# Kernel tuning notes

Hardware: AMD Instinct MI355X
Metric: run time of the kernel (lower is better)

## Reference

```python
import jax, jax.numpy as jnp
import numpy as np

B, S, DK = 32, 2048, 64

def setup_inputs() -> dict:
    key = jax.random.key(0)
    kq, kk, kv = jax.random.split(key, 3)
    Q = jax.random.normal(kq, (B, S, DK), dtype=jnp.float32)
    K = jax.random.normal(kk, (B, S, DK), dtype=jnp.float32)
    V = jax.random.normal(kv, (B, S, DK), dtype=jnp.float32)
    return {"Q": Q, "K": K, "V": V}

def reference(Q, K, V):
    # attn_scores = Q K^T / sqrt(d_k); full [B,S,S] probs materialized (naive, non-flash)
    d_k = Q.shape[-1]
    scores = jnp.einsum('bqd,bkd->bqk', Q, K) / jnp.sqrt(jnp.asarray(d_k, Q.dtype))
    probs = jax.nn.softmax(scores, axis=-1)
    return jnp.einsum('bqk,bkd->bqd', probs, V)
```

## Files before the change

kernel.cpp:

```cpp
#include <hip/hip_runtime.h>
#include <hip/hip_bf16.h>

#define BATCH 32
#define SEQ   2048
#define DKK   64

constexpr int QT  = 128;
constexpr int KT  = 64;
constexpr int NIT = SEQ / KT;
constexpr int LST = 66;

typedef __attribute__((ext_vector_type(8)))  short bf16x8;
typedef __attribute__((ext_vector_type(16))) float f32x16;
typedef __attribute__((ext_vector_type(2)))  unsigned uint2v;

__device__ __forceinline__ unsigned cvt2(float a, float b) {
    union { __hip_bfloat162 h; unsigned u; } c;
    c.h = __float22bfloat162_rn(make_float2(a, b));
    return c.u;
}

__device__ __forceinline__ float fast_exp2(float x) {
#if __has_builtin(__builtin_amdgcn_exp2f)
    return __builtin_amdgcn_exp2f(x);
#else
    return exp2f(x);
#endif
}

__global__ __launch_bounds__(256, 2) void attn_fwd(
        const float* __restrict__ Q, const float* __restrict__ K,
        const float* __restrict__ V, float* __restrict__ O) {
    __shared__ short Kb[2][KT][LST];
    __shared__ short Vt[2][DKK][LST];

    const int tid  = threadIdx.x;
    const int w    = tid >> 6;
    const int lane = tid & 63;
    const int hi   = lane >> 5;
    const int l31  = lane & 31;

    const int lin  = (int)blockIdx.x + ((int)blockIdx.y << 4);
    const int work = ((lin & 7) << 6) | (lin >> 3);
    const int b    = work >> 4;
    const int q0   = (work & 15) * QT + w * 32;

    const float qscale = 0.125f * 1.44269504088896340736f;
    bf16x8 qfrag[4];
    #pragma unroll
    for (int c = 0; c < 4; ++c) {
        const float* qp = Q + ((size_t)b * SEQ + q0 + l31) * DKK + 16*c + 8*hi;
        float4 a  = *(const float4*)qp;
        float4 a2 = *(const float4*)(qp + 4);
        union { bf16x8 v; unsigned u[4]; } f;
        f.u[0] = cvt2(a.x*qscale,  a.y*qscale);
        f.u[1] = cvt2(a.z*qscale,  a.w*qscale);
        f.u[2] = cvt2(a2.x*qscale, a2.y*qscale);
        f.u[3] = cvt2(a2.z*qscale, a2.w*qscale);
        qfrag[c] = f.v;
    }

    f32x16 o0 = {}, o1 = {};
    float ls0 = 0.f, ls1 = 0.f, ls2 = 0.f, ls3 = 0.f;

    const float* Kbase = K + (size_t)b * SEQ * DKK;
    const float* Vbase = V + (size_t)b * SEQ * DKK;

    const int krow0 = tid >> 4;
    const int kcol  = (tid & 15) << 2;
    const int vd    = tid & 63;
    const int vg    = (tid >> 6) << 4;

    float4 kp[4];
    float  vp[16];
    auto load_regs = [&](int t) {
        const float* Kg = Kbase + (size_t)(t * KT) * DKK;
        #pragma unroll
        for (int i = 0; i < 4; ++i)
            kp[i] = *(const float4*)(Kg + (size_t)(krow0 + 16*i) * DKK + kcol);
        const float* Vg = Vbase + (size_t)(t * KT + vg) * DKK + vd;
        #pragma unroll
        for (int i = 0; i < 16; ++i) vp[i] = Vg[(size_t)i * DKK];
    };
    auto write_lds = [&](int buf) {
        #pragma unroll
        for (int i = 0; i < 4; ++i) {
            int2 kk;
            kk.x = (int)cvt2(kp[i].x, kp[i].y);
            kk.y = (int)cvt2(kp[i].z, kp[i].w);
            *(int2*)&Kb[buf][krow0 + 16*i][kcol] = kk;
        }
        union { bf16x8 v; unsigned u[4]; } t0, t1;
        t0.u[0] = cvt2(vp[0],  vp[1]);  t0.u[1] = cvt2(vp[2],  vp[3]);
        t0.u[2] = cvt2(vp[4],  vp[5]);  t0.u[3] = cvt2(vp[6],  vp[7]);
        t1.u[0] = cvt2(vp[8],  vp[9]);  t1.u[1] = cvt2(vp[10], vp[11]);
        t1.u[2] = cvt2(vp[12], vp[13]); t1.u[3] = cvt2(vp[14], vp[15]);
        *(bf16x8*)&Vt[buf][vd][vg]     = t0.v;
        *(bf16x8*)&Vt[buf][vd][vg + 8] = t1.v;
    };

    load_regs(0);
    write_lds(0);
    load_regs(1);
    __syncthreads();

    for (int it = 0; it < NIT; ++it) {
        const int cur = it & 1;

        #pragma unroll
        for (int kt2 = 0; kt2 < 2; ++kt2) {
            f32x16 acc = {};
            __builtin_amdgcn_s_setprio(1);
            #pragma unroll
            for (int c = 0; c < 4; ++c) {
                bf16x8 kf = *(const bf16x8*)&Kb[cur][32*kt2 + l31][16*c + 8*hi];
                acc = __builtin_amdgcn_mfma_f32_32x32x16_bf16(kf, qfrag[c], acc, 0, 0, 0);
            }
            __builtin_amdgcn_s_setprio(0);

            float p[16];
            #pragma unroll
            for (int r = 0; r < 16; r += 4) {
                p[r]   = fast_exp2(acc[r]);   ls0 += p[r];
                p[r+1] = fast_exp2(acc[r+1]); ls1 += p[r+1];
                p[r+2] = fast_exp2(acc[r+2]); ls2 += p[r+2];
                p[r+3] = fast_exp2(acc[r+3]); ls3 += p[r+3];
            }

            unsigned pw0 = cvt2(p[0],  p[1]),  pw1 = cvt2(p[2],  p[3]);
            unsigned pw2 = cvt2(p[4],  p[5]),  pw3 = cvt2(p[6],  p[7]);
            unsigned pw4 = cvt2(p[8],  p[9]),  pw5 = cvt2(p[10], p[11]);
            unsigned pw6 = cvt2(p[12], p[13]), pw7 = cvt2(p[14], p[15]);
            uint2v s02 = __builtin_amdgcn_permlane32_swap(pw0, pw2, false, false);
            uint2v s13 = __builtin_amdgcn_permlane32_swap(pw1, pw3, false, false);
            uint2v s46 = __builtin_amdgcn_permlane32_swap(pw4, pw6, false, false);
            uint2v s57 = __builtin_amdgcn_permlane32_swap(pw5, pw7, false, false);
            union { bf16x8 v; unsigned u[4]; } pa0, pa1;
            pa0.u[0] = s02[0]; pa0.u[1] = s13[0]; pa0.u[2] = s02[1]; pa0.u[3] = s13[1];
            pa1.u[0] = s46[0]; pa1.u[1] = s57[0]; pa1.u[2] = s46[1]; pa1.u[3] = s57[1];

            __builtin_amdgcn_s_setprio(1);
            #pragma unroll
            for (int cc = 0; cc < 2; ++cc) {
                const int c = 2*kt2 + cc;
                bf16x8 pf  = cc ? pa1.v : pa0.v;
                bf16x8 vf0 = *(const bf16x8*)&Vt[cur][l31     ][16*c + 8*hi];
                bf16x8 vf1 = *(const bf16x8*)&Vt[cur][32 + l31][16*c + 8*hi];
                o0 = __builtin_amdgcn_mfma_f32_32x32x16_bf16(vf0, pf, o0, 0, 0, 0);
                o1 = __builtin_amdgcn_mfma_f32_32x32x16_bf16(vf1, pf, o1, 0, 0, 0);
            }
            __builtin_amdgcn_s_setprio(0);
        }

        if (it + 1 < NIT) {
            write_lds(1 - cur);
            if (it + 2 < NIT) load_regs(it + 2);
            asm volatile("s_waitcnt lgkmcnt(0)" ::: "memory");
            __builtin_amdgcn_s_barrier();
        }
    }

    float s = (ls0 + ls1) + (ls2 + ls3);
    s += __shfl_xor(s, 32);
    const float inv = 1.0f / s;

    float* op = O + ((size_t)b * SEQ + q0 + l31) * DKK;
    #pragma unroll
    for (int G = 0; G < 4; ++G) {
        float4 st;
        st.x = o0[4*G + 0] * inv; st.y = o0[4*G + 1] * inv;
        st.z = o0[4*G + 2] * inv; st.w = o0[4*G + 3] * inv;
        *(float4*)(op + 8*G + 4*hi) = st;
        st.x = o1[4*G + 0] * inv; st.y = o1[4*G + 1] * inv;
        st.z = o1[4*G + 2] * inv; st.w = o1[4*G + 3] * inv;
        *(float4*)(op + 32 + 8*G + 4*hi) = st;
    }
}

extern "C" void kernel_launch(void* const* d_in, const int* in_sizes, int n_in,
                              void* d_out, int out_size, void* d_ws, size_t ws_size,
                              hipStream_t stream) {
    const float* Q = (const float*)d_in[0];
    const float* K = (const float*)d_in[1];
    const float* V = (const float*)d_in[2];
    float* O = (float*)d_out;
    dim3 grid(SEQ / QT, BATCH);
    attn_fwd<<<grid, dim3(256), 0, stream>>>(Q, K, V, O);
}
```

Before: 136.0 us.

## Precompute bf16 K and transposed V in a prep kernel, double KV tile

Adds a prep kernel that converts K to bf16 and writes V as a bf16 transposed [B,D,S] array into the workspace. The attention kernel then loads pre-converted 16-byte vectors straight into LDS, with no per-block fp32 conversion or strided V gathers. The KV tile grows from 64 to 128 keys. In the original each of the 16 query blocks per batch reloaded and reconverted the fp32 K/V. The cost is an extra kernel launch, a workspace round trip and more LDS per block, which may affect occupancy.

New measurement: 137.6 us. Within noise of the previous version (+1.2%).

```diff
diff --git a/kernel.cpp b/kernel.cpp
--- a/kernel.cpp
+++ b/kernel.cpp
@@ -6,9 +6,10 @@
 #define DKK   64
 
 constexpr int QT  = 128;
-constexpr int KT  = 64;
+constexpr int KT  = 128;
 constexpr int NIT = SEQ / KT;
-constexpr int LST = 66;
+constexpr int LSK = 66;
+constexpr int LSV = 130;
 
 typedef __attribute__((ext_vector_type(8)))  short bf16x8;
 typedef __attribute__((ext_vector_type(16))) float f32x16;
@@ -18,6 +19,12 @@
     union { __hip_bfloat162 h; unsigned u; } c;
     c.h = __float22bfloat162_rn(make_float2(a, b));
     return c.u;
+}
+
+__device__ __forceinline__ unsigned short b16u(float x) {
+    union { __hip_bfloat16 h; unsigned short u; } t;
+    t.h = __float2bfloat16(x);
+    return t.u;
 }
 
 __device__ __forceinline__ float fast_exp2(float x) {
@@ -28,11 +35,56 @@
 #endif
 }
 
+__global__ __launch_bounds__(256) void prep_kv(
+        const float* __restrict__ K, const float* __restrict__ V,
+        unsigned short* __restrict__ K16, unsigned short* __restrict__ V16) {
+    __shared__ unsigned short T[64][66];
+    const int b   = blockIdx.y;
+    const int k0  = blockIdx.x << 6;
+    const int tid = threadIdx.x;
+    const int r   = tid >> 2;
+    const int c   = (tid & 3) << 4;
+
+    {
+        const float* kp = K + ((size_t)b * SEQ + k0 + r) * DKK + c;
+        float4 a0 = *(const float4*)(kp + 0);
+        float4 a1 = *(const float4*)(kp + 4);
+        float4 a2 = *(const float4*)(kp + 8);
+        float4 a3 = *(const float4*)(kp + 12);
+        union { bf16x8 v; unsigned u[4]; } w0, w1;
+        w0.u[0] = cvt2(a0.x, a0.y); w0.u[1] = cvt2(a0.z, a0.w);
+        w0.u[2] = cvt2(a1.x, a1.y); w0.u[3] = cvt2(a1.z, a1.w);
+        w1.u[0] = cvt2(a2.x, a2.y); w1.u[1] = cvt2(a2.z, a2.w);
+        w1.u[2] = cvt2(a3.x, a3.y); w1.u[3] = cvt2(a3.z, a3.w);
+        unsigned short* kd = K16 + ((size_t)b * SEQ + k0 + r) * DKK + c;
+        *(bf16x8*)(kd)     = w0.v;
+        *(bf16x8*)(kd + 8) = w1.v;
+    }
+    {
+        const float* vp = V + ((size_t)b * SEQ + k0 + r) * DKK + c;
+        float4 a0 = *(const float4*)(vp + 0);
+        float4 a1 = *(const float4*)(vp + 4);
+        float4 a2 = *(const float4*)(vp + 8);
+        float4 a3 = *(const float4*)(vp + 12);
+        const float f[16] = {a0.x,a0.y,a0.z,a0.w, a1.x,a1.y,a1.z,a1.w,
+                             a2.x,a2.y,a2.z,a2.w, a3.x,a3.y,a3.z,a3.w};
+        #pragma unroll
+        for (int j = 0; j < 16; ++j) T[c + j][r] = b16u(f[j]);
+        __syncthreads();
+        unsigned short* vd = V16 + ((size_t)b * DKK + r) * SEQ + k0 + c;
+        union { bf16x8 v; unsigned short s[8]; } o0, o1;
+        #pragma unroll
+        for (int j = 0; j < 8; ++j) { o0.s[j] = T[r][c + j]; o1.s[j] = T[r][c + 8 + j]; }
+        *(bf16x8*)(vd)     = o0.v;
+        *(bf16x8*)(vd + 8) = o1.v;
+    }
+}
+
 __global__ __launch_bounds__(256, 2) void attn_fwd(
-        const float* __restrict__ Q, const float* __restrict__ K,
-        const float* __restrict__ V, float* __restrict__ O) {
-    __shared__ short Kb[2][KT][LST];
-    __shared__ short Vt[2][DKK][LST];
+        const float* __restrict__ Q, const unsigned short* __restrict__ K16,
+        const unsigned short* __restrict__ V16, float* __restrict__ O) {
+    __shared__ short Kb[2][KT][LSK];
+    __shared__ short Vt[2][DKK][LSV];
 
     const int tid  = threadIdx.x;
     const int w    = tid >> 6;
@@ -63,40 +115,34 @@
     f32x16 o0 = {}, o1 = {};
     float ls0 = 0.f, ls1 = 0.f, ls2 = 0.f, ls3 = 0.f;
 
-    const float* Kbase = K + (size_t)b * SEQ * DKK;
-    const float* Vbase = V + (size_t)b * SEQ * DKK;
-
-    const int krow0 = tid >> 4;
-    const int kcol  = (tid & 15) << 2;
-    const int vd    = tid & 63;
-    const int vg    = (tid >> 6) << 4;
-
-    float4 kp[4];
-    float  vp[16];
+    const unsigned short* Kbase = K16 + (size_t)b * SEQ * DKK;
+    const unsigned short* Vbase = V16 + (size_t)b * DKK * SEQ;
+
+    const int sr = tid >> 3;
+    const int sc = (tid & 7) << 3;
+
+    bf16x8 kreg[4], vreg[4];
     auto load_regs = [&](int t) {
-        const float* Kg = Kbase + (size_t)(t * KT) * DKK;
+        const unsigned short* Kg = Kbase + (size_t)(t * KT) * DKK + sc;
         #pragma unroll
         for (int i = 0; i < 4; ++i)
-            kp[i] = *(const float4*)(Kg + (size_t)(krow0 + 16*i) * DKK + kcol);
-        const float* Vg = Vbase + (size_t)(t * KT + vg) * DKK + vd;
-        #pragma unroll
-        for (int i = 0; i < 16; ++i) vp[i] = Vg[(size_t)i * DKK];
+            kreg[i] = *(const bf16x8*)(Kg + (size_t)(sr + 32*i) * DKK);
+        const unsigned short* Vg = Vbase + (size_t)sr * SEQ + t * KT + sc;
+        #pragma unroll
+        for (int i = 0; i < 2; ++i) {
+            vreg[2*i]     = *(const bf16x8*)(Vg + (size_t)(32*i) * SEQ);
+            vreg[2*i + 1] = *(const bf16x8*)(Vg + (size_t)(32*i) * SEQ + 64);
+        }
     };
     auto write_lds = [&](int buf) {
         #pragma unroll
-        for (int i = 0; i < 4; ++i) {
-            int2 kk;
-            kk.x = (int)cvt2(kp[i].x, kp[i].y);
-            kk.y = (int)cvt2(kp[i].z, kp[i].w);
-            *(int2*)&Kb[buf][krow0 + 16*i][kcol] = kk;
-        }
-        union { bf16x8 v; unsigned u[4]; } t0, t1;
-        t0.u[0] = cvt2(vp[0],  vp[1]);  t0.u[1] = cvt2(vp[2],  vp[3]);
-        t0.u[2] = cvt2(vp[4],  vp[5]);  t0.u[3] = cvt2(vp[6],  vp[7]);
-        t1.u[0] = cvt2(vp[8],  vp[9]);  t1.u[1] = cvt2(vp[10], vp[11]);
-        t1.u[2] = cvt2(vp[12], vp[13]); t1.u[3] = cvt2(vp[14], vp[15]);
-        *(bf16x8*)&Vt[buf][vd][vg]     = t0.v;
-        *(bf16x8*)&Vt[buf][vd][vg + 8] = t1.v;
+        for (int i = 0; i < 4; ++i)
+            *(bf16x8*)&Kb[buf][sr + 32*i][sc] = kreg[i];
+        #pragma unroll
+        for (int i = 0; i < 2; ++i) {
+            *(bf16x8*)&Vt[buf][sr + 32*i][sc]      = vreg[2*i];
+            *(bf16x8*)&Vt[buf][sr + 32*i][sc + 64] = vreg[2*i + 1];
+        }
     };
 
     load_regs(0);
@@ -108,13 +154,13 @@
         const int cur = it & 1;
 
         #pragma unroll
-        for (int kt2 = 0; kt2 < 2; ++kt2) {
+        for (int kt2 = 0; kt2 < 4; ++kt2) {
             f32x16 acc = {};
             __builtin_amdgcn_s_setprio(1);
             #pragma unroll
-            for (int c = 0; c < 4; ++c) {
-                bf16x8 kf = *(const bf16x8*)&Kb[cur][32*kt2 + l31][16*c + 8*hi];
-                acc = __builtin_amdgcn_mfma_f32_32x32x16_bf16(kf, qfrag[c], acc, 0, 0, 0);
+            for (int cd = 0; cd < 4; ++cd) {
+                bf16x8 kf = *(const bf16x8*)&Kb[cur][32*kt2 + l31][16*cd + 8*hi];
+                acc = __builtin_amdgcn_mfma_f32_32x32x16_bf16(kf, qfrag[cd], acc, 0, 0, 0);
             }
             __builtin_amdgcn_s_setprio(0);
 
@@ -184,6 +230,11 @@
     const float* K = (const float*)d_in[1];
     const float* V = (const float*)d_in[2];
     float* O = (float*)d_out;
+
+    unsigned short* K16 = (unsigned short*)d_ws;
+    unsigned short* V16 = K16 + (size_t)BATCH * SEQ * DKK;
+
+    prep_kv<<<dim3(SEQ / 64, BATCH), dim3(256), 0, stream>>>(K, V, K16, V16);
     dim3 grid(SEQ / QT, BATCH);
-    attn_fwd<<<grid, dim3(256), 0, stream>>>(Q, K, V, O);
-}
+    attn_fwd<<<grid, dim3(256), 0, stream>>>(Q, K16, V16, O);
+}
```
